# Kernel optimization log

Hardware: AMD Instinct MI355X
Metric: run time of the kernel (lower is better)

The kernel has to match this reference:

```python
import jax, jax.numpy as jnp
import numpy as np

N_EXPERTS = 8
Z_DIM = 128
HID = 1024
OUT = 3072  # e.g. 3x32x32 flattened generator output
BATCH = 2048


def hash_vectors(z, n):
    """Deterministic per-sample hash -> expert index in [0, n).

    Proxy for the repo's hash_vectors (which hashes the latent vector):
    quantize |z|, sum over feature dim, mod n. Non-differentiable by design.
    """
    return jnp.mod(jnp.floor(jnp.abs(z) * 1000.0).sum(axis=1).astype(jnp.int32), n)


def setup_inputs() -> dict:
    key = jax.random.key(0)
    kz, k1, kb1, k2, kb2 = jax.random.split(key, 5)
    z = jax.random.normal(kz, (BATCH, Z_DIM), dtype=jnp.float32)
    s1 = 1.0 / np.sqrt(Z_DIM)
    s2 = 1.0 / np.sqrt(HID)
    # Stacked per-expert MLP params (each expert independently initialized,
    # mirroring reset_parameters on each deepcopy).
    W1 = jax.random.uniform(k1, (N_EXPERTS, Z_DIM, HID), jnp.float32, -s1, s1)
    b1 = jax.random.uniform(kb1, (N_EXPERTS, HID), jnp.float32, -s1, s1)
    W2 = jax.random.uniform(k2, (N_EXPERTS, HID, OUT), jnp.float32, -s2, s2)
    b2 = jax.random.uniform(kb2, (N_EXPERTS, OUT), jnp.float32, -s2, s2)
    return {"z": z, "W1": W1, "b1": b1, "W2": W2, "b2": b2}


def reference(z, W1, b1, W2, b2):
    # Hard routing: each sample i goes to expert idx[i].
    idx = hash_vectors(z, N_EXPERTS)  # [B]
    # Dense compute-all-experts then select (vectorized replacement for the
    # per-sample Python loop in the original forward).
    h = jax.nn.relu(jnp.einsum('bi,eih->beh', z, W1) + b1[None, :, :])  # [B,E,H]
    y = jnp.einsum('beh,eho->beo', h, W2) + b2[None, :, :]              # [B,E,O]
    out = jnp.take_along_axis(y, idx[:, None, None], axis=1)[:, 0, :]   # [B,O]
    return out
```

## Files before the change

kernel.cpp:

```cpp
#include <hip/hip_runtime.h>
#include <hip/hip_bf16.h>


#define BATCH 2048
#define ZD 128
#define HID 1024
#define OUTD 3072
#define NEXP 8

#define TMG 128
#define TNG 128
#define BKG 64
#define MAXTF 24

typedef short bf16x8 __attribute__((ext_vector_type(8)));
typedef float f32x4 __attribute__((ext_vector_type(4)));


__global__ __launch_bounds__(256) void route_kernel(const float* __restrict__ z,
                                                    __hip_bfloat16* __restrict__ zb,
                                                    int* counts, int* bucket) {
    __shared__ int lcnt[NEXP];
    __shared__ int gbase[NEXP];
    int t = threadIdx.x;
    if (t < NEXP) lcnt[t] = 0;
    __syncthreads();

    int s = blockIdx.x * 32 + (t >> 3);
    int li = t & 7;
    const float* zp = z + (size_t)s * ZD + li * 16;
    float sum = 0.f;
    union { bf16x8 v8; __hip_bfloat16 h[8]; } u0, u1;
#pragma unroll
    for (int i = 0; i < 4; i++) {
        float4 v = ((const float4*)zp)[i];
        sum += floorf(fabsf(v.x) * 1000.0f) + floorf(fabsf(v.y) * 1000.0f) +
               floorf(fabsf(v.z) * 1000.0f) + floorf(fabsf(v.w) * 1000.0f);
        __hip_bfloat16* dst = (i < 2) ? &u0.h[i * 4] : &u1.h[(i - 2) * 4];
        dst[0] = __float2bfloat16(v.x);
        dst[1] = __float2bfloat16(v.y);
        dst[2] = __float2bfloat16(v.z);
        dst[3] = __float2bfloat16(v.w);
    }
    bf16x8* zo = (bf16x8*)(zb + (size_t)s * ZD + li * 16);
    zo[0] = u0.v8;
    zo[1] = u1.v8;

    sum += __shfl_down(sum, 4);
    sum += __shfl_down(sum, 2);
    sum += __shfl_down(sum, 1);
    int e = 0, lpos = 0;
    if (li == 0) {
        e = ((int)sum) & 7;
        lpos = atomicAdd(&lcnt[e], 1);
    }
    __syncthreads();
    if (t < NEXP) gbase[t] = atomicAdd(&counts[t], lcnt[t]);
    __syncthreads();
    if (li == 0) bucket[e * BATCH + gbase[e] + lpos] = s;
}

__global__ void scan_kernel(const int* __restrict__ counts, int* ntl,
                            int* texp, int* perm, const int* __restrict__ bucket) {
    __shared__ int soff[NEXP + 1];
    __shared__ int scnt[NEXP];
    if (threadIdx.x == 0) {
        int o = 0;
        for (int e = 0; e < NEXP; e++) {
            scnt[e] = counts[e];
            soff[e] = o;
            o += (scnt[e] + TMG - 1) & ~(TMG - 1);
        }
        soff[NEXP] = o;
        *ntl = o / TMG;
    }
    __syncthreads();
    int total = soff[NEXP];
    for (int r = threadIdx.x; r < total; r += blockDim.x) {
        int e = 0;
        while (r >= soff[e + 1]) e++;
        int i = r - soff[e];
        perm[r] = (i < scnt[e]) ? bucket[e * BATCH + i] : -1;
        if ((r & (TMG - 1)) == 0) texp[r / TMG] = e;
    }
}


__global__ __launch_bounds__(256, 3) void gemm1_fast(
    const __hip_bfloat16* __restrict__ zb, const float* __restrict__ W1,
    const float* __restrict__ b1, const int* __restrict__ ntl,
    const int* __restrict__ texp, const int* __restrict__ perm,
    __hip_bfloat16* __restrict__ H) {
    int mt = blockIdx.y;
    if (mt >= *ntl) return;
    int e = texp[mt];
    int n0 = blockIdx.x * TNG;

    __shared__ __align__(16) __hip_bfloat16 As[TMG * BKG];
    __shared__ __align__(16) __hip_bfloat16 Bs[TNG * BKG];
    __shared__ int rows_s[TMG];

    int tid = threadIdx.x;
    if (tid < TMG) rows_s[tid] = perm[mt * TMG + tid];
    __syncthreads();

    int lane = tid & 63, wave = tid >> 6;
    int cc = lane & 15, q = lane >> 4;
    int mw = (wave >> 1) * 64, nw = (wave & 1) * 64;

    int sr = tid >> 3, sc = tid & 7;
    int awbase = sr * 64 + (sc ^ (sr & 7)) * 8;
    const __hip_bfloat16* Arp[4];
#pragma unroll
    for (int p = 0; p < 4; p++) {
        int r = rows_s[p * 32 + sr];
        if (r < 0) r = 0;
        Arp[p] = zb + (size_t)r * ZD + sc * 8;
    }
    int bkc = tid & 7, bn = (tid >> 3) * 4;
    const float* Bgf = W1 + (size_t)e * ZD * HID + (size_t)(bkc * 8) * HID + n0 + bn;
    int bwb[4];
#pragma unroll
    for (int j = 0; j < 4; j++)
        bwb[j] = (bn + j) * 64 + ((bkc ^ ((bn + j) & 7))) * 8;

    int A0 = (mw + cc) * 64, B0 = (nw + cc) * 64;
    int X0 = (q ^ (cc & 7)) * 8, X1 = ((4 + q) ^ (cc & 7)) * 8;

    float bias[4];
#pragma unroll
    for (int j = 0; j < 4; j++) bias[j] = b1[(size_t)e * HID + n0 + nw + j * 16 + cc];

    f32x4 zero4 = {0.f, 0.f, 0.f, 0.f};
    f32x4 acc[4][4];
#pragma unroll
    for (int i = 0; i < 4; i++)
#pragma unroll
        for (int j = 0; j < 4; j++) acc[i][j] = zero4;

    bf16x8 ga[4];
    union { bf16x8 v8; __hip_bfloat16 h[8]; } gb[4];
#pragma unroll
    for (int p = 0; p < 4; p++) ga[p] = *(const bf16x8*)(Arp[p]);
#pragma unroll
    for (int i = 0; i < 8; i++) {
        float4 v = *(const float4*)(Bgf + (size_t)i * HID);
        gb[0].h[i] = __float2bfloat16(v.x);
        gb[1].h[i] = __float2bfloat16(v.y);
        gb[2].h[i] = __float2bfloat16(v.z);
        gb[3].h[i] = __float2bfloat16(v.w);
    }
#pragma unroll
    for (int it = 0; it < ZD / BKG; ++it) {
        __syncthreads();
#pragma unroll
        for (int p = 0; p < 4; p++) *(bf16x8*)(As + awbase + p * 2048) = ga[p];
#pragma unroll
        for (int j = 0; j < 4; j++) *(bf16x8*)(Bs + bwb[j]) = gb[j].v8;
        __syncthreads();
        if (it + 1 < ZD / BKG) {
#pragma unroll
            for (int p = 0; p < 4; p++)
                ga[p] = *(const bf16x8*)(Arp[p] + (it + 1) * BKG);
#pragma unroll
            for (int i = 0; i < 8; i++) {
                float4 v = *(const float4*)(Bgf + (size_t)((it + 1) * BKG + i) * HID);
                gb[0].h[i] = __float2bfloat16(v.x);
                gb[1].h[i] = __float2bfloat16(v.y);
                gb[2].h[i] = __float2bfloat16(v.z);
                gb[3].h[i] = __float2bfloat16(v.w);
            }
        }
#pragma unroll
        for (int kh = 0; kh < 2; ++kh) {
            int X = kh ? X1 : X0;
            bf16x8 af[4], bfr[4];
#pragma unroll
            for (int i = 0; i < 4; i++) af[i] = *(const bf16x8*)(As + A0 + i * 1024 + X);
#pragma unroll
            for (int j = 0; j < 4; j++) bfr[j] = *(const bf16x8*)(Bs + B0 + j * 1024 + X);
#pragma unroll
            for (int i = 0; i < 4; i++)
#pragma unroll
                for (int j = 0; j < 4; j++)
                    acc[i][j] = __builtin_amdgcn_mfma_f32_16x16x32_bf16(af[i], bfr[j],
                                                                        acc[i][j], 0, 0, 0);
        }
    }
#pragma unroll
    for (int i = 0; i < 4; i++)
#pragma unroll
        for (int r = 0; r < 4; r++) {
            int m = mw + i * 16 + q * 4 + r;
            __hip_bfloat16* hp = H + (size_t)(mt * TMG + m) * HID + n0 + nw + cc;
#pragma unroll
            for (int j = 0; j < 4; j++)
                hp[j * 16] = __float2bfloat16(fmaxf(acc[i][j][r] + bias[j], 0.f));
        }
}

__global__ __launch_bounds__(256, 3) void gemm2_fast(
    const __hip_bfloat16* __restrict__ H, const float* __restrict__ W2,
    const float* __restrict__ b2, const int* __restrict__ ntl,
    const int* __restrict__ texp, const int* __restrict__ perm,
    float* __restrict__ out) {
    int mt = blockIdx.y;
    if (mt >= *ntl) return;
    int e = texp[mt];
    int n0 = blockIdx.x * TNG;

    __shared__ __align__(16) __hip_bfloat16 As[TMG * BKG];
    __shared__ __align__(16) __hip_bfloat16 Bs[TNG * BKG];
    __shared__ int rows_s[TMG];

    int tid = threadIdx.x;
    if (tid < TMG) rows_s[tid] = perm[mt * TMG + tid];

    int lane = tid & 63, wave = tid >> 6;
    int cc = lane & 15, q = lane >> 4;
    int mw = (wave >> 1) * 64, nw = (wave & 1) * 64;

    int sr = tid >> 3, sc = tid & 7;
    int awbase = sr * 64 + (sc ^ (sr & 7)) * 8;
    const __hip_bfloat16* Ag = H + ((size_t)mt * TMG + sr) * HID + sc * 8;
    int bkc = tid & 7, bn = (tid >> 3) * 4;
    const float* Bgf = W2 + (size_t)e * HID * OUTD + (size_t)(bkc * 8) * OUTD + n0 + bn;
    int bwb[4];
#pragma unroll
    for (int j = 0; j < 4; j++)
        bwb[j] = (bn + j) * 64 + ((bkc ^ ((bn + j) & 7))) * 8;

    int A0 = (mw + cc) * 64, B0 = (nw + cc) * 64;
    int X0 = (q ^ (cc & 7)) * 8, X1 = ((4 + q) ^ (cc & 7)) * 8;

    float bias[4];
#pragma unroll
    for (int j = 0; j < 4; j++) bias[j] = b2[(size_t)e * OUTD + n0 + nw + j * 16 + cc];

    f32x4 zero4 = {0.f, 0.f, 0.f, 0.f};
    f32x4 acc[4][4];
#pragma unroll
    for (int i = 0; i < 4; i++)
#pragma unroll
        for (int j = 0; j < 4; j++) acc[i][j] = zero4;

    bf16x8 ga[4];
    union { bf16x8 v8; __hip_bfloat16 h[8]; } gb[4];
#pragma unroll
    for (int p = 0; p < 4; p++) ga[p] = *(const bf16x8*)(Ag + (size_t)p * 32 * HID);
#pragma unroll
    for (int i = 0; i < 8; i++) {
        float4 v = *(const float4*)(Bgf + (size_t)i * OUTD);
        gb[0].h[i] = __float2bfloat16(v.x);
        gb[1].h[i] = __float2bfloat16(v.y);
        gb[2].h[i] = __float2bfloat16(v.z);
        gb[3].h[i] = __float2bfloat16(v.w);
    }
    for (int it = 0; it < HID / BKG; ++it) {
        __syncthreads();
#pragma unroll
        for (int p = 0; p < 4; p++) *(bf16x8*)(As + awbase + p * 2048) = ga[p];
#pragma unroll
        for (int j = 0; j < 4; j++) *(bf16x8*)(Bs + bwb[j]) = gb[j].v8;
        __syncthreads();
        if (it + 1 < HID / BKG) {
            int k1 = (it + 1) * BKG;
#pragma unroll
            for (int p = 0; p < 4; p++)
                ga[p] = *(const bf16x8*)(Ag + (size_t)p * 32 * HID + k1);
#pragma unroll
            for (int i = 0; i < 8; i++) {
                float4 v = *(const float4*)(Bgf + (size_t)(k1 + i) * OUTD);
                gb[0].h[i] = __float2bfloat16(v.x);
                gb[1].h[i] = __float2bfloat16(v.y);
                gb[2].h[i] = __float2bfloat16(v.z);
                gb[3].h[i] = __float2bfloat16(v.w);
            }
        }
#pragma unroll
        for (int kh = 0; kh < 2; ++kh) {
            int X = kh ? X1 : X0;
            bf16x8 af[4], bfr[4];
#pragma unroll
            for (int i = 0; i < 4; i++) af[i] = *(const bf16x8*)(As + A0 + i * 1024 + X);
#pragma unroll
            for (int j = 0; j < 4; j++) bfr[j] = *(const bf16x8*)(Bs + B0 + j * 1024 + X);
#pragma unroll
            for (int i = 0; i < 4; i++)
#pragma unroll
                for (int j = 0; j < 4; j++)
                    acc[i][j] = __builtin_amdgcn_mfma_f32_16x16x32_bf16(af[i], bfr[j],
                                                                        acc[i][j], 0, 0, 0);
        }
    }
#pragma unroll
    for (int i = 0; i < 4; i++)
#pragma unroll
        for (int r = 0; r < 4; r++) {
            int m = mw + i * 16 + q * 4 + r;
            int orow = rows_s[m];
            if (orow >= 0) {
                float* op = out + (size_t)orow * OUTD + n0 + nw + cc;
#pragma unroll
                for (int j = 0; j < 4; j++) op[j * 16] = acc[i][j][r] + bias[j];
            }
        }
}

extern "C" void kernel_launch(void* const* d_in, const int* in_sizes, int n_in,
                              void* d_out, int out_size, void* d_ws, size_t ws_size,
                              hipStream_t stream) {
    const float* z  = (const float*)d_in[0];
    const float* W1 = (const float*)d_in[1];
    const float* b1 = (const float*)d_in[2];
    const float* W2 = (const float*)d_in[3];
    const float* b2 = (const float*)d_in[4];
    float* out = (float*)d_out;

    char* ws = (char*)d_ws;
    int* counts = (int*)ws;
    int* ntl    = (int*)(ws + 64);
    int* texp   = (int*)(ws + 128);
    int* perm   = (int*)(ws + 256);
    int* bucket = (int*)(ws + 12544);
    __hip_bfloat16* zb  = (__hip_bfloat16*)(ws + 78080);
    __hip_bfloat16* Hb  = (__hip_bfloat16*)(ws + 602368);

    hipMemsetAsync(counts, 0, 64, stream);
    hipLaunchKernelGGL(route_kernel, dim3(BATCH / 32), dim3(256), 0, stream,
                       z, zb, counts, bucket);
    hipLaunchKernelGGL(scan_kernel, dim3(1), dim3(256), 0, stream,
                       counts, ntl, texp, perm, bucket);
    hipLaunchKernelGGL(gemm1_fast, dim3(HID / TNG, MAXTF), dim3(256), 0, stream,
                       zb, W1, b1, ntl, texp, perm, Hb);
    hipLaunchKernelGGL(gemm2_fast, dim3(OUTD / TNG, MAXTF), dim3(256), 0, stream,
                       Hb, W2, b2, ntl, texp, perm, out);
}
```

Before: 218.2 us.

## Double-buffer LDS in gemm2 and defer W2 bf16 conversion past loads

The second expert GEMM now ping-pongs between two shared-memory tile buffers, so each iteration needs one barrier instead of two. Raw fp32 W2 values are held in registers and converted to bf16 only at the start of the next iteration, which keeps the global loads in flight longer. The extra LDS and register use lower the launch bound from three blocks per CU to two, trading occupancy for latency hiding.

Result: faster. 202.4 us (-7.2%).

```diff
diff --git a/kernel.cpp b/kernel.cpp
--- a/kernel.cpp
+++ b/kernel.cpp
@@ -85,7 +85,6 @@
     }
 }
 
-
 __global__ __launch_bounds__(256, 3) void gemm1_fast(
     const __hip_bfloat16* __restrict__ zb, const float* __restrict__ W1,
     const float* __restrict__ b1, const int* __restrict__ ntl,
@@ -199,7 +198,7 @@
         }
 }
 
-__global__ __launch_bounds__(256, 3) void gemm2_fast(
+__global__ __launch_bounds__(256, 2) void gemm2_fast(
     const __hip_bfloat16* __restrict__ H, const float* __restrict__ W2,
     const float* __restrict__ b2, const int* __restrict__ ntl,
     const int* __restrict__ texp, const int* __restrict__ perm,
@@ -209,8 +208,8 @@
     int e = texp[mt];
     int n0 = blockIdx.x * TNG;
 
-    __shared__ __align__(16) __hip_bfloat16 As[TMG * BKG];
-    __shared__ __align__(16) __hip_bfloat16 Bs[TNG * BKG];
+    __shared__ __align__(16) __hip_bfloat16 As[2][TMG * BKG];
+    __shared__ __align__(16) __hip_bfloat16 Bs[2][TNG * BKG];
     __shared__ int rows_s[TMG];
 
     int tid = threadIdx.x;
@@ -245,46 +244,46 @@
         for (int j = 0; j < 4; j++) acc[i][j] = zero4;
 
     bf16x8 ga[4];
-    union { bf16x8 v8; __hip_bfloat16 h[8]; } gb[4];
+    float4 braw[8];
 #pragma unroll
     for (int p = 0; p < 4; p++) ga[p] = *(const bf16x8*)(Ag + (size_t)p * 32 * HID);
 #pragma unroll
-    for (int i = 0; i < 8; i++) {
-        float4 v = *(const float4*)(Bgf + (size_t)i * OUTD);
-        gb[0].h[i] = __float2bfloat16(v.x);
-        gb[1].h[i] = __float2bfloat16(v.y);
-        gb[2].h[i] = __float2bfloat16(v.z);
-        gb[3].h[i] = __float2bfloat16(v.w);
-    }
-    for (int it = 0; it < HID / BKG; ++it) {
-        __syncthreads();
-#pragma unroll
-        for (int p = 0; p < 4; p++) *(bf16x8*)(As + awbase + p * 2048) = ga[p];
-#pragma unroll
-        for (int j = 0; j < 4; j++) *(bf16x8*)(Bs + bwb[j]) = gb[j].v8;
-        __syncthreads();
-        if (it + 1 < HID / BKG) {
+    for (int i = 0; i < 8; i++) braw[i] = *(const float4*)(Bgf + (size_t)i * OUTD);
+
+    const int NIT = HID / BKG;
+    for (int it = 0; it < NIT; ++it) {
+        __hip_bfloat16* Ac = As[it & 1];
+        __hip_bfloat16* Bc = Bs[it & 1];
+        union { bf16x8 v8; __hip_bfloat16 h[8]; } gb[4];
+#pragma unroll
+        for (int i = 0; i < 8; i++) {
+            gb[0].h[i] = __float2bfloat16(braw[i].x);
+            gb[1].h[i] = __float2bfloat16(braw[i].y);
+            gb[2].h[i] = __float2bfloat16(braw[i].z);
+            gb[3].h[i] = __float2bfloat16(braw[i].w);
+        }
+#pragma unroll
+        for (int p = 0; p < 4; p++) *(bf16x8*)(Ac + awbase + p * 2048) = ga[p];
+#pragma unroll
+        for (int j = 0; j < 4; j++) *(bf16x8*)(Bc + bwb[j]) = gb[j].v8;
+        if (it + 1 < NIT) {
             int k1 = (it + 1) * BKG;
 #pragma unroll
             for (int p = 0; p < 4; p++)
                 ga[p] = *(const bf16x8*)(Ag + (size_t)p * 32 * HID + k1);
 #pragma unroll
-            for (int i = 0; i < 8; i++) {
-                float4 v = *(const float4*)(Bgf + (size_t)(k1 + i) * OUTD);
-                gb[0].h[i] = __float2bfloat16(v.x);
-                gb[1].h[i] = __float2bfloat16(v.y);
-                gb[2].h[i] = __float2bfloat16(v.z);
-                gb[3].h[i] = __float2bfloat16(v.w);
-            }
-        }
+            for (int i = 0; i < 8; i++)
+                braw[i] = *(const float4*)(Bgf + (size_t)(k1 + i) * OUTD);
+        }
+        __syncthreads();
 #pragma unroll
         for (int kh = 0; kh < 2; ++kh) {
             int X = kh ? X1 : X0;
             bf16x8 af[4], bfr[4];
 #pragma unroll
-            for (int i = 0; i < 4; i++) af[i] = *(const bf16x8*)(As + A0 + i * 1024 + X);
-#pragma unroll
-            for (int j = 0; j < 4; j++) bfr[j] = *(const bf16x8*)(Bs + B0 + j * 1024 + X);
+            for (int i = 0; i < 4; i++) af[i] = *(const bf16x8*)(Ac + A0 + i * 1024 + X);
+#pragma unroll
+            for (int j = 0; j < 4; j++) bfr[j] = *(const bf16x8*)(Bc + B0 + j * 1024 + X);
 #pragma unroll
             for (int i = 0; i < 4; i++)
 #pragma unroll
```
